# Kernel optimization log

Measured on AMD Instinct MI355X. Metric: run time of the kernel, lower is better.

Reference implementation:

```python
import jax, jax.numpy as jnp
import numpy as np
import math

H = 8        # num_heads
DK = 64      # key_dim
DV = 64      # value_dim
FACTOR = 4


def setup_inputs() -> dict:
    key = jax.random.key(0)
    B, T, S, D = 4, 2048, 2048, 512
    Dout = H * DV
    ks = jax.random.split(key, 16)
    sample_k = min(int(FACTOR * math.log(S)), S)  # = 33
    inp = {
        "x_q": jax.random.normal(ks[0], (B, T, D), jnp.float32),
        "x_k": jax.random.normal(ks[1], (B, S, D), jnp.float32),
        "x_v": jax.random.normal(ks[2], (B, S, D), jnp.float32),
        "Wq": jax.random.normal(ks[3], (D, H * DK), jnp.float32) * 0.02,
        "bq": jnp.zeros((H * DK,), jnp.float32),
        "Wk": jax.random.normal(ks[4], (D, H * DK), jnp.float32) * 0.02,
        "bk": jnp.zeros((H * DK,), jnp.float32),
        "Wv": jax.random.normal(ks[5], (D, H * DV), jnp.float32) * 0.02,
        "bv": jnp.zeros((H * DV,), jnp.float32),
        "Wo": jax.random.normal(ks[6], (H * DV, Dout), jnp.float32) * 0.02,
        "bo": jnp.zeros((Dout,), jnp.float32),
        "index_sample": jax.random.randint(ks[7], (T, sample_k), 0, S, jnp.int32),
    }
    return inp


def reference(x_q, x_k, x_v, Wq, bq, Wk, bk, Wv, bv, Wo, bo, index_sample):
    B, T, D = x_q.shape
    S = x_k.shape[1]
    u = min(int(FACTOR * math.log(T)), T)  # n_top queries kept

    q = (x_q @ Wq + bq).reshape(B, T, H, DK)
    k = (x_k @ Wk + bk).reshape(B, S, H, DK)
    v = (x_v @ Wv + bv).reshape(B, S, H, DV)

    # --- _prob_QK: sampled QK to score queries ---
    ks = k[:, index_sample]                                  # [B,T,J,H,dk]
    qk_s = jnp.einsum('bthd,btjhd->bthj', q, ks)             # [B,T,H,J]
    M = qk_s.max(-1) - qk_s.mean(-1)                         # [B,T,H]
    _, top = jax.lax.top_k(jnp.transpose(M, (0, 2, 1)), u)   # [B,H,u]

    b_idx = jnp.arange(B)[:, None, None]
    h_idx = jnp.arange(H)[None, :, None]
    q_red = q[b_idx, top, h_idx]                             # [B,H,u,dk]
    qk = jnp.einsum('bhud,bshd->bhus', q_red, k)             # [B,H,u,S]

    # --- s0: default (no mask) context = mean of values over S ---
    ctx = jnp.broadcast_to(v.mean(axis=1, keepdims=True), (B, T, H, DV))
    ctx = jnp.transpose(ctx, (0, 2, 1, 3))                   # [B,H,T,dv]

    # --- s1: scaled softmax over full keys for top queries ---
    scores = jax.nn.softmax(qk * (1.0 / math.sqrt(DK)), axis=-1)
    attn = jnp.einsum('bhus,bshd->bhud', scores, v)          # [B,H,u,dv]

    # --- scatter top-query results into context / scores ---
    ctx = ctx.at[b_idx, h_idx, top].set(attn)                # [B,H,T,dv]
    final_scores = jnp.full((B, H, T, S), 1.0 / S, dtype=scores.dtype)
    final_scores = final_scores.at[b_idx, h_idx, top].set(scores)

    out = jnp.transpose(ctx, (0, 2, 1, 3)).reshape(B, T, H * DV)
    out = out @ Wo + bo                                      # [B,T,output_dim]
    return out, final_scores
```

## Files before the change

kernel.cpp:

```cpp
#include <hip/hip_runtime.h>

typedef __attribute__((ext_vector_type(8))) short short8;
typedef __attribute__((ext_vector_type(4))) float f32x4;

constexpr int Bn  = 4;
constexpr int Tn  = 2048;
constexpr int Sn  = 2048;
constexpr int Dn  = 512;
constexpr int Hn  = 8;
constexpr int DKn = 64;
constexpr int DVn = 64;
constexpr int HDn = 512;
constexpr int SKn = 30;
constexpr int Un  = 30;
constexpr int Gu  = 2;
constexpr int NGroups = Un / Gu;
constexpr int NAttnG  = Bn * Hn * NGroups;
constexpr int NOutF   = (Bn * Tn) / 8;
constexpr int NGemm  = 768;
constexpr float kScale = 0.125f;

constexpr int NWsplit = 192;
constexpr int NVPart  = 64;
constexpr int NSampled = Bn * Tn;

constexpr int NFillG = 9216;
constexpr int NFillS = 2048;
constexpr int NFillT = 5120;
constexpr int FillRowsG = 0;
constexpr int FillRowsS = NFillG * 4;
constexpr int FillRowsT = (NFillG + NFillS) * 4;

__device__ __forceinline__ ushort bf16_rne(float x) {
  unsigned u = __float_as_uint(x);
  return (ushort)((u + 0x7fffu + ((u >> 16) & 1u)) >> 16);
}
__device__ __forceinline__ float bf16f(ushort h) {
  return __uint_as_float(((unsigned)h) << 16);
}
__device__ __forceinline__ void nt_store4(f32x4* p, f32x4 v) {
  __builtin_nontemporal_store(v, p);
}
__device__ __forceinline__ void fill_rows4_256(float* fscores, size_t r0, int tid) {
  const float c = 1.0f / Sn;
  const f32x4 c4v = {c, c, c, c};
  f32x4* fs4 = (f32x4*)fscores + r0 * (Sn / 4);
#pragma unroll
  for (int i = 0; i < 8; ++i) nt_store4(fs4 + i * 256 + tid, c4v);
}
__device__ __forceinline__ void gload_lds16(const void* g, void* lds) {
  __builtin_amdgcn_global_load_lds((const __attribute__((address_space(1))) void*)g,
                                   (__attribute__((address_space(3))) void*)lds, 16, 0, 0);
}

#define MFMA(accv, av, bv) \
  asm volatile("v_mfma_f32_16x16x32_bf16 %0, %1, %2, %0" : "+v"(accv) : "v"(av), "v"(bv))

__global__ __launch_bounds__(256) void prep_split_kernel(
    const float* __restrict__ Wq, const float* __restrict__ Wk, const float* __restrict__ Wv,
    ushort* __restrict__ WtH, ushort* __restrict__ WtL) {
  const int tid = threadIdx.x;
  const int bid = blockIdx.x;

  const int z = bid / 64, t = bid % 64;
  const int k0 = (t >> 3) * 64, n0 = (t & 7) * 64;
  const float* W = (z == 0) ? Wq : (z == 1) ? Wk : Wv;
  __shared__ float tile[64][65];
  const int r = tid >> 2, c0 = (tid & 3) * 16;
#pragma unroll
  for (int i = 0; i < 16; i += 4) {
    const float4 vv = *(const float4*)(W + (size_t)(k0 + r) * HDn + n0 + c0 + i);
    tile[r][c0 + i] = vv.x; tile[r][c0 + i + 1] = vv.y;
    tile[r][c0 + i + 2] = vv.z; tile[r][c0 + i + 3] = vv.w;
  }
  __syncthreads();
  unsigned hp[8], lp[8];
#pragma unroll
  for (int i = 0; i < 16; i += 2) {
    const float x0 = tile[c0 + i][r];
    const float x1 = tile[c0 + i + 1][r];
    const ushort h0 = bf16_rne(x0), h1 = bf16_rne(x1);
    const ushort l0 = bf16_rne(x0 - bf16f(h0)), l1 = bf16_rne(x1 - bf16f(h1));
    hp[i >> 1] = (unsigned)h0 | ((unsigned)h1 << 16);
    lp[i >> 1] = (unsigned)l0 | ((unsigned)l1 << 16);
  }
  const size_t off = (size_t)(z * 512 + n0 + r) * 512 + k0 + c0;
  *(uint4*)(WtH + off)     = make_uint4(hp[0], hp[1], hp[2], hp[3]);
  *(uint4*)(WtH + off + 8) = make_uint4(hp[4], hp[5], hp[6], hp[7]);
  *(uint4*)(WtL + off)     = make_uint4(lp[0], lp[1], lp[2], lp[3]);
  *(uint4*)(WtL + off + 8) = make_uint4(lp[4], lp[5], lp[6], lp[7]);
}

__global__ __launch_bounds__(256, 2) void gemm_fill_kernel(
    const float* __restrict__ xq, const float* __restrict__ xk, const float* __restrict__ xv,
    const ushort* __restrict__ WtH, const ushort* __restrict__ WtL,
    const float* __restrict__ bq, const float* __restrict__ bk, const float* __restrict__ bv,
    float* __restrict__ qo, float* __restrict__ ko, float* __restrict__ vo,
    float* __restrict__ fscores) {
  const int bid = blockIdx.x;
  const int tid = threadIdx.x;

  if (bid >= NGemm) {
    fill_rows4_256(fscores, (size_t)FillRowsG + (size_t)(bid - NGemm) * 4, tid);
    return;
  }

  __shared__ ushort AsH[64][32];
  __shared__ ushort AsL[64][32];
  __shared__ ushort BsH[256][32];
  __shared__ ushort BsL[256][32];

  const int z = bid >> 8;
  const int rem = bid & 255;
  const int bm = (rem >> 1) * 64;
  const int bn = (rem & 1) * 256;
  const float* X = (z == 0) ? xq : (z == 1) ? xk : xv;
  const float* bias = (z == 0) ? bq : (z == 1) ? bk : bv;
  float* Y = (z == 0) ? qo : (z == 1) ? ko : vo;

  const int lane = tid & 63;
  const int wave = tid >> 6;
  const int fr = lane & 15;
  const int gk = lane >> 4;

  const int ar = tid >> 2, ag = tid & 3;
  const float* xrow = X + (size_t)(bm + ar) * Dn + ag * 8;
  const int agq = (ag ^ ((ar >> 1) & 3)) * 8;

  const int gsrc = (lane & 3) ^ ((lane >> 3) & 3);
  const ushort* bgH = WtH + (size_t)(z * 512 + bn + wave * 64 + (lane >> 2)) * 512 + gsrc * 8;
  const ushort* bgL = WtL + (size_t)(z * 512 + bn + wave * 64 + (lane >> 2)) * 512 + gsrc * 8;
  ushort* ldsH0 = &BsH[wave * 64][0];
  ushort* ldsL0 = &BsL[wave * 64][0];

  const int gq = (gk ^ ((fr >> 1) & 3)) * 8;

  f32x4 acc[4][4];
#pragma unroll
  for (int m = 0; m < 4; ++m)
#pragma unroll
    for (int n = 0; n < 4; ++n)
#pragma unroll
      for (int j = 0; j < 4; ++j) acc[m][n][j] = 0.f;

  float4 af0 = *(const float4*)(xrow + 0);
  float4 af1 = *(const float4*)(xrow + 4);

  for (int k0 = 0; k0 < Dn; k0 += 32) {
    __syncthreads();
#pragma unroll
    for (int c = 0; c < 4; ++c) {
      gload_lds16(bgH + k0 + c * 8192, ldsH0 + c * 512);
      gload_lds16(bgL + k0 + c * 8192, ldsL0 + c * 512);
    }
    {
      float xf[8] = {af0.x, af0.y, af0.z, af0.w, af1.x, af1.y, af1.z, af1.w};
      unsigned hp[4], lp[4];
#pragma unroll
      for (int i = 0; i < 8; i += 2) {
        const ushort h0 = bf16_rne(xf[i]), h1 = bf16_rne(xf[i + 1]);
        const ushort l0 = bf16_rne(xf[i] - bf16f(h0)), l1 = bf16_rne(xf[i + 1] - bf16f(h1));
        hp[i >> 1] = (unsigned)h0 | ((unsigned)h1 << 16);
        lp[i >> 1] = (unsigned)l0 | ((unsigned)l1 << 16);
      }
      *(uint4*)&AsH[ar][agq] = make_uint4(hp[0], hp[1], hp[2], hp[3]);
      *(uint4*)&AsL[ar][agq] = make_uint4(lp[0], lp[1], lp[2], lp[3]);
    }
    if (k0 + 32 < Dn) {
      af0 = *(const float4*)(xrow + k0 + 32);
      af1 = *(const float4*)(xrow + k0 + 36);
    }
    __syncthreads();

    short8 aH[4], aL[4], bH[4], bL[4];
#pragma unroll
    for (int m = 0; m < 4; ++m) {
      aH[m] = *(const short8*)&AsH[m * 16 + fr][gq];
      aL[m] = *(const short8*)&AsL[m * 16 + fr][gq];
    }
#pragma unroll
    for (int n = 0; n < 4; ++n) {
      bH[n] = *(const short8*)&BsH[wave * 64 + n * 16 + fr][gq];
      bL[n] = *(const short8*)&BsL[wave * 64 + n * 16 + fr][gq];
    }
#pragma unroll
    for (int m = 0; m < 4; ++m)
#pragma unroll
      for (int n = 0; n < 4; ++n) {
        MFMA(acc[m][n], aH[m], bH[n]);
        MFMA(acc[m][n], aH[m], bL[n]);
        MFMA(acc[m][n], aL[m], bH[n]);
      }
  }
  asm volatile("s_nop 7\n\ts_nop 7");

  float bsv[4];
#pragma unroll
  for (int n = 0; n < 4; ++n) bsv[n] = bias[bn + wave * 64 + n * 16 + fr];
#pragma unroll
  for (int m = 0; m < 4; ++m) {
#pragma unroll
    for (int n = 0; n < 4; ++n) {
      const int col = bn + wave * 64 + n * 16 + fr;
#pragma unroll
      for (int j = 0; j < 4; ++j) {
        Y[(size_t)(bm + m * 16 + gk * 4 + j) * HDn + col] = acc[m][n][j] + bsv[n];
      }
    }
  }
}

__global__ __launch_bounds__(64) void sampled_m_kernel(
    const float* __restrict__ q, const float* __restrict__ k,
    const int* __restrict__ idxs, float* __restrict__ Mt,
    const float* __restrict__ v, float* __restrict__ vpart,
    float* __restrict__ fscores) {
  const int bid = blockIdx.x;
  const int lane = threadIdx.x;

  if (bid >= NVPart + NSampled) {
    const size_t r0 = (size_t)FillRowsS + (size_t)(bid - NVPart - NSampled) * 4;
    const float c = 1.0f / Sn;
    const f32x4 c4v = {c, c, c, c};
    f32x4* p = (f32x4*)fscores + r0 * (Sn / 4);
#pragma unroll
    for (int i = 0; i < 32; ++i) nt_store4(p + i * 64 + lane, c4v);
    return;
  }

  if (bid < NVPart) {
    const int pb = bid;
    const int b = pb >> 4, part = pb & 15;
    const float4* v4 = (const float4*)(v + (size_t)b * Sn * HDn);
    float4 a0 = make_float4(0.f, 0.f, 0.f, 0.f);
    float4 a1 = make_float4(0.f, 0.f, 0.f, 0.f);
    const int s0 = part * 128;
    for (int s = s0; s < s0 + 128; ++s) {
      const float4 x0 = v4[(size_t)s * 128 + lane * 2];
      const float4 x1 = v4[(size_t)s * 128 + lane * 2 + 1];
      a0.x += x0.x; a0.y += x0.y; a0.z += x0.z; a0.w += x0.w;
      a1.x += x1.x; a1.y += x1.y; a1.z += x1.z; a1.w += x1.w;
    }
    float4* vp4 = (float4*)vpart + (size_t)pb * 128;
    vp4[lane * 2] = a0; vp4[lane * 2 + 1] = a1;
    return;
  }

  const int inner = bid - NVPart;
  const int b = inner >> 11, t = inner & (Tn - 1);

  const int* idxt = idxs + t * SKn;
  const float* qrow = q + ((size_t)(b * Tn + t)) * HDn + lane * 8;
  const float4 qv0 = *(const float4*)qrow;
  const float4 qv1 = *(const float4*)(qrow + 4);
  const float* kb = k + (size_t)b * Sn * HDn + lane * 8;

  float mx = -1e30f, sum = 0.f;
#pragma unroll 6
  for (int j = 0; j < SKn; ++j) {
    const float* kr = kb + (size_t)idxt[j] * HDn;
    const float4 kv0 = *(const float4*)kr;
    const float4 kv1 = *(const float4*)(kr + 4);
    float p = kv0.x * qv0.x + kv0.y * qv0.y + kv0.z * qv0.z + kv0.w * qv0.w
            + kv1.x * qv1.x + kv1.y * qv1.y + kv1.z * qv1.z + kv1.w * qv1.w;
    p += __shfl_xor(p, 1);
    p += __shfl_xor(p, 2);
    p += __shfl_xor(p, 4);
    mx = fmaxf(mx, p);
    sum += p;
  }
  if ((lane & 7) == 0) {
    const int h = lane >> 3;
    Mt[((size_t)(b * Hn + h)) * Tn + t] = mx - sum * (1.0f / SKn);
  }
}

__global__ __launch_bounds__(256) void topk_vmean_base_kernel(
    const float* __restrict__ Mt, const float* __restrict__ vpart,
    const float* __restrict__ Wo, const float* __restrict__ bo,
    int* __restrict__ top, float* __restrict__ vmean, float* __restrict__ basep,
    float* __restrict__ fscores) {
  const int tid = threadIdx.x;
  const int lane = tid & 63, w = tid >> 6;

  if (blockIdx.x >= 36) {
    fill_rows4_256(fscores, (size_t)FillRowsT + (size_t)(blockIdx.x - 36) * 4, tid);
    return;
  }

  __shared__ float vals[Tn];
  __shared__ float wv[4];
  __shared__ int wi[4];
  __shared__ float4 part[256];
  __shared__ float vm[HDn];

  if (blockIdx.x < 32) {
    const int bh = blockIdx.x;
    for (int i = tid; i < Tn; i += 256) vals[i] = Mt[(size_t)bh * Tn + i];
    __syncthreads();
    for (int u = 0; u < Un; ++u) {
      float bv = -1e30f; int bi = 0x7fffffff;
      for (int i = tid; i < Tn; i += 256) {
        const float x = vals[i];
        if (x > bv) { bv = x; bi = i; }
      }
#pragma unroll
      for (int o = 1; o < 64; o <<= 1) {
        const float ov = __shfl_xor(bv, o);
        const int oi = __shfl_xor(bi, o);
        if (ov > bv || (ov == bv && oi < bi)) { bv = ov; bi = oi; }
      }
      if (lane == 0) { wv[w] = bv; wi[w] = bi; }
      __syncthreads();
      bv = wv[0]; bi = wi[0];
#pragma unroll
      for (int j = 1; j < 4; ++j) {
        if (wv[j] > bv || (wv[j] == bv && wi[j] < bi)) { bv = wv[j]; bi = wi[j]; }
      }
      if (tid == 0) { top[bh * Un + u] = bi; vals[bi] = -1e30f; }
      __syncthreads();
    }
  } else {
    const int b = blockIdx.x - 32;
    const int c4 = tid & 127, half = tid >> 7;
    float4 acc = make_float4(0.f, 0.f, 0.f, 0.f);
    for (int p = half * 8; p < half * 8 + 8; ++p) {
      const float4 x = ((const float4*)vpart)[(size_t)(b * 16 + p) * 128 + c4];
      acc.x += x.x; acc.y += x.y; acc.z += x.z; acc.w += x.w;
    }
    part[tid] = acc;
    __syncthreads();
    if (half == 0) {
      float4 a = part[c4], bpp = part[128 + c4];
      const float sc = 1.0f / Sn;
      float4 r = make_float4((a.x + bpp.x) * sc, (a.y + bpp.y) * sc,
                             (a.z + bpp.z) * sc, (a.w + bpp.w) * sc);
      *(float4*)(vm + c4 * 4) = r;
      *(float4*)(vmean + b * HDn + c4 * 4) = r;
    }
    __syncthreads();
    const float4* Wo4 = (const float4*)Wo;
    float4 acc2 = make_float4(0.f, 0.f, 0.f, 0.f);
    for (int c = half * 256; c < half * 256 + 256; ++c) {
      const float vmc = vm[c];
      const float4 wrow = Wo4[(size_t)c * 128 + c4];
      acc2.x += vmc * wrow.x; acc2.y += vmc * wrow.y;
      acc2.z += vmc * wrow.z; acc2.w += vmc * wrow.w;
    }
    __syncthreads();
    part[tid] = acc2;
    __syncthreads();
    if (half == 0) {
      float4 a = part[c4], bpp = part[128 + c4];
      const float4 bb = ((const float4*)bo)[c4];
      float4 r = make_float4(a.x + bpp.x + bb.x, a.y + bpp.y + bb.y,
                             a.z + bpp.z + bb.z, a.w + bpp.w + bb.w);
      ((float4*)basep)[b * 128 + c4] = r;
    }
  }
}

__global__ __launch_bounds__(256) void attn_out_kernel(
    const float* __restrict__ q, const float* __restrict__ k,
    const float* __restrict__ v, const float* __restrict__ vmean,
    const int* __restrict__ top, const float* __restrict__ Wo,
    const float* __restrict__ basep,
    float* __restrict__ out, float* __restrict__ fscores) {
  const int tid = threadIdx.x;
  const int bid = blockIdx.x;

  if (bid >= NAttnG) {
    const int fid = bid - NAttnG;
    const int r0 = fid * 8;
    const int b = r0 >> 11;
    const int t0 = r0 & (Tn - 1);
    __shared__ int sflag8[8];
    if (tid < 8) sflag8[tid] = 0;
    __syncthreads();
    if (tid < Hn * Un) {
      const int d = top[b * Hn * Un + tid] - t0;
      if (d >= 0 && d < 8) sflag8[d] = 1;
    }
    __syncthreads();
    const int col4 = tid & 127, rh = tid >> 7;
    const float4 bv4 = ((const float4*)basep)[b * 128 + col4];
    const f32x4 bvx = {bv4.x, bv4.y, bv4.z, bv4.w};
#pragma unroll
    for (int rp = 0; rp < 4; ++rp) {
      const int rr = rp * 2 + rh;
      float4* orow4 = (float4*)(out + (size_t)(r0 + rr) * HDn) + col4;
      if (sflag8[rr]) {
        float* p = (float*)orow4;
        atomicAdd(p + 0, bv4.x); atomicAdd(p + 1, bv4.y);
        atomicAdd(p + 2, bv4.z); atomicAdd(p + 3, bv4.w);
      } else {
        nt_store4((f32x4*)orow4, bvx);
      }
    }
    return;
  }

  const int xs = bid & 7;
  const int b = xs & 3;
  const int combo = (bid >> 3) + (xs >> 2) * 60;
  const int h = combo / NGroups;
  const int grp = combo % NGroups;
  const int bh = b * Hn + h;
  const int u0 = grp * Gu;
  const int lane = tid & 63, w = tid >> 6;

  __shared__ float qs[Gu][DKn];
  __shared__ float sc[Gu][2052];
  __shared__ float red[8];
  __shared__ int tsel[Gu];
  __shared__ float4 partv[4][Gu][16];

  if (tid < Gu) tsel[tid] = top[bh * Un + u0 + tid];
  __syncthreads();
  if (tid < Gu * DKn) {
    const int g = tid >> 6, d = tid & 63;
    qs[g][d] = q[((size_t)(b * Tn + tsel[g])) * HDn + h * DKn + d];
  }
  __syncthreads();

  const float4* k4 = (const float4*)k;
  for (int s = tid; s < Sn; s += 256) {
    const float4* krow = k4 + ((size_t)(b * Sn + s)) * 128 + h * 16;
    float acc[Gu];
#pragma unroll
    for (int g = 0; g < Gu; ++g) acc[g] = 0.f;
#pragma unroll
    for (int d4i = 0; d4i < 16; ++d4i) {
      const float4 kv = krow[d4i];
#pragma unroll
      for (int g = 0; g < Gu; ++g) {
        const float4 qv = *(const float4*)&qs[g][d4i * 4];
        acc[g] += kv.x * qv.x + kv.y * qv.y + kv.z * qv.z + kv.w * qv.w;
      }
    }
#pragma unroll
    for (int g = 0; g < Gu; ++g) sc[g][s] = acc[g] * kScale;
  }
  __syncthreads();

  float invs[Gu];
#pragma unroll
  for (int g = 0; g < Gu; ++g) {
    float lm = -1e30f;
    for (int i = tid; i < Sn; i += 256) lm = fmaxf(lm, sc[g][i]);
#pragma unroll
    for (int o = 1; o < 64; o <<= 1) lm = fmaxf(lm, __shfl_xor(lm, o));
    if (lane == 0) red[w] = lm;
    __syncthreads();
    const float mx = fmaxf(fmaxf(red[0], red[1]), fmaxf(red[2], red[3]));
    float ls = 0.f;
    for (int i = tid; i < Sn; i += 256) {
      const float e = __expf(sc[g][i] - mx);
      sc[g][i] = e;
      ls += e;
    }
#pragma unroll
    for (int o = 1; o < 64; o <<= 1) ls += __shfl_xor(ls, o);
    if (lane == 0) red[4 + w] = ls;
    __syncthreads();
    invs[g] = 1.0f / (red[4] + red[5] + red[6] + red[7]);
    __syncthreads();
  }
#pragma unroll
  for (int g = 0; g < Gu; ++g) {
    const float inv = invs[g];
    float4* scg4 = (float4*)sc[g];
    f32x4* fsrow4 = (f32x4*)(fscores + ((size_t)bh * Tn + tsel[g]) * Sn);
#pragma unroll
    for (int it = 0; it < 2; ++it) {
      const int i = it * 256 + tid;
      float4 p = scg4[i];
      p.x *= inv; p.y *= inv; p.z *= inv; p.w *= inv;
      scg4[i] = p;
      const f32x4 px = {p.x, p.y, p.z, p.w};
      nt_store4(fsrow4 + i, px);
    }
  }
  __syncthreads();

  const int d4 = lane & 15;
  const int sg = (w << 2) + (lane >> 4);
  const float4* v4 = (const float4*)v;
  float4 pacc[Gu];
#pragma unroll
  for (int g = 0; g < Gu; ++g) pacc[g] = make_float4(0.f, 0.f, 0.f, 0.f);
  for (int s = sg; s < Sn; s += 16) {
    const float4 vv = v4[((size_t)(b * Sn + s)) * 128 + h * 16 + d4];
#pragma unroll
    for (int g = 0; g < Gu; ++g) {
      const float p = sc[g][s];
      pacc[g].x += p * vv.x; pacc[g].y += p * vv.y;
      pacc[g].z += p * vv.z; pacc[g].w += p * vv.w;
    }
  }
#pragma unroll
  for (int g = 0; g < Gu; ++g) {
#pragma unroll
    for (int o = 16; o < 64; o <<= 1) {
      pacc[g].x += __shfl_xor(pacc[g].x, o);
      pacc[g].y += __shfl_xor(pacc[g].y, o);
      pacc[g].z += __shfl_xor(pacc[g].z, o);
      pacc[g].w += __shfl_xor(pacc[g].w, o);
    }
    if (lane < 16) partv[w][g][lane] = pacc[g];
  }
  __syncthreads();
  if (tid < Gu * 16) {
    const int g = tid >> 4, dd = tid & 15;
    float4 r = partv[0][g][dd];
    const float4 r1 = partv[1][g][dd], r2 = partv[2][g][dd], r3 = partv[3][g][dd];
    r.x += r1.x + r2.x + r3.x; r.y += r1.y + r2.y + r3.y;
    r.z += r1.z + r2.z + r3.z; r.w += r1.w + r2.w + r3.w;
    const float4 vm4 = ((const float4*)vmean)[bh * 16 + dd];
    r.x -= vm4.x; r.y -= vm4.y; r.z -= vm4.z; r.w -= vm4.w;
    *(float4*)&qs[g][dd * 4] = r;
  }
  __syncthreads();

  const int col4 = tid & 127, g = tid >> 7;
  const float4* Wo4 = (const float4*)Wo;
  {
    float4 a = make_float4(0.f, 0.f, 0.f, 0.f);
#pragma unroll
    for (int d = 0; d < DKn; ++d) {
      const float dv = qs[g][d];
      const float4 wrow = Wo4[(size_t)(h * DKn + d) * 128 + col4];
      a.x += dv * wrow.x; a.y += dv * wrow.y;
      a.z += dv * wrow.z; a.w += dv * wrow.w;
    }
    float* orow = out + ((size_t)(b * Tn + tsel[g])) * HDn + col4 * 4;
    atomicAdd(orow + 0, a.x); atomicAdd(orow + 1, a.y);
    atomicAdd(orow + 2, a.z); atomicAdd(orow + 3, a.w);
  }
}

extern "C" void kernel_launch(void* const* d_in, const int* in_sizes, int n_in,
                              void* d_out, int out_size, void* d_ws, size_t ws_size,
                              hipStream_t stream) {
  const float* x_q = (const float*)d_in[0];
  const float* x_k = (const float*)d_in[1];
  const float* x_v = (const float*)d_in[2];
  const float* Wq = (const float*)d_in[3];
  const float* bq = (const float*)d_in[4];
  const float* Wk = (const float*)d_in[5];
  const float* bk = (const float*)d_in[6];
  const float* Wv = (const float*)d_in[7];
  const float* bv = (const float*)d_in[8];
  const float* Wo = (const float*)d_in[9];
  const float* bo = (const float*)d_in[10];
  const int* idx = (const int*)d_in[11];

  float* out = (float*)d_out;
  float* fscores = out + (size_t)Bn * Tn * HDn;

  float* ws = (float*)d_ws;
  float* q = ws;
  float* kp = ws + (size_t)4194304;
  float* vp = ws + (size_t)8388608;
  float* Mt = ws + (size_t)12582912;
  float* vmean = ws + (size_t)12648448;
  float* basep = ws + (size_t)12650496;
  int* top = (int*)(ws + (size_t)12652544);
  float* vpart = ws + (size_t)12656640;

  char* scr = (char*)(fscores + (size_t)49152 * Sn);
  ushort* WtH = (ushort*)scr;
  ushort* WtL = WtH + (size_t)3 * 512 * 512;

  prep_split_kernel<<<NWsplit, 256, 0, stream>>>(Wq, Wk, Wv, WtH, WtL);

  gemm_fill_kernel<<<NGemm + NFillG, 256, 0, stream>>>(
      x_q, x_k, x_v, WtH, WtL, bq, bk, bv, q, kp, vp, fscores);

  sampled_m_kernel<<<NVPart + NSampled + NFillS, 64, 0, stream>>>(
      q, kp, idx, Mt, vp, vpart, fscores);

  topk_vmean_base_kernel<<<36 + NFillT, 256, 0, stream>>>(
      Mt, vpart, Wo, bo, top, vmean, basep, fscores);

  attn_out_kernel<<<NAttnG + NOutF, 256, 0, stream>>>(
      q, kp, vp, vmean, top, Wo, basep, out, fscores);
}
```

Baseline: 752.4 us.

## Use one top query per attention block and register-resident two-stage top-k

Result: slower. 786.3 us (+4.5%).

```diff
diff --git a/kernel.cpp b/kernel.cpp
--- a/kernel.cpp
+++ b/kernel.cpp
@@ -13,8 +13,7 @@
 constexpr int HDn = 512;
 constexpr int SKn = 30;
 constexpr int Un  = 30;
-constexpr int Gu  = 2;
-constexpr int NGroups = Un / Gu;
+constexpr int NGroups = Un;
 constexpr int NAttnG  = Bn * Hn * NGroups;
 constexpr int NOutF   = (Bn * Tn) / 8;
 constexpr int NGemm  = 768;
@@ -24,9 +23,9 @@
 constexpr int NVPart  = 64;
 constexpr int NSampled = Bn * Tn;
 
-constexpr int NFillG = 9216;
+constexpr int NFillG = 10240;
 constexpr int NFillS = 2048;
-constexpr int NFillT = 5120;
+constexpr int NFillT = 4096;
 constexpr int FillRowsG = 0;
 constexpr int FillRowsS = NFillG * 4;
 constexpr int FillRowsT = (NFillG + NFillS) * 4;
@@ -288,37 +287,60 @@
     return;
   }
 
-  __shared__ float vals[Tn];
-  __shared__ float wv[4];
-  __shared__ int wi[4];
+  __shared__ float cval[128];
+  __shared__ int cidx[128];
   __shared__ float4 part[256];
   __shared__ float vm[HDn];
 
   if (blockIdx.x < 32) {
     const int bh = blockIdx.x;
-    for (int i = tid; i < Tn; i += 256) vals[i] = Mt[(size_t)bh * Tn + i];
-    __syncthreads();
+    if (tid < 128) { cval[tid] = -1e30f; cidx[tid] = -1; }
+    __syncthreads();
+    const float* mrow = Mt + (size_t)bh * Tn;
+    const int base = w * 512 + lane;
+    float rv[8];
+#pragma unroll
+    for (int j = 0; j < 8; ++j) rv[j] = mrow[base + j * 64];
     for (int u = 0; u < Un; ++u) {
-      float bv = -1e30f; int bi = 0x7fffffff;
-      for (int i = tid; i < Tn; i += 256) {
-        const float x = vals[i];
-        if (x > bv) { bv = x; bi = i; }
-      }
+      float bv = rv[0]; int bj = 0;
+#pragma unroll
+      for (int j = 1; j < 8; ++j) {
+        if (rv[j] > bv) { bv = rv[j]; bj = j; }
+      }
+      int bi = base + bj * 64;
 #pragma unroll
       for (int o = 1; o < 64; o <<= 1) {
         const float ov = __shfl_xor(bv, o);
         const int oi = __shfl_xor(bi, o);
         if (ov > bv || (ov == bv && oi < bi)) { bv = ov; bi = oi; }
       }
-      if (lane == 0) { wv[w] = bv; wi[w] = bi; }
-      __syncthreads();
-      bv = wv[0]; bi = wi[0];
-#pragma unroll
-      for (int j = 1; j < 4; ++j) {
-        if (wv[j] > bv || (wv[j] == bv && wi[j] < bi)) { bv = wv[j]; bi = wi[j]; }
-      }
-      if (tid == 0) { top[bh * Un + u] = bi; vals[bi] = -1e30f; }
-      __syncthreads();
+      if (((bi >> 9) == w) && ((bi & 63) == lane)) {
+        const int bj2 = (bi >> 6) & 7;
+#pragma unroll
+        for (int j = 0; j < 8; ++j) {
+          if (j == bj2) rv[j] = -1e30f;
+        }
+      }
+      if (lane == 0) { cval[w * 32 + u] = bv; cidx[w * 32 + u] = bi; }
+    }
+    __syncthreads();
+    if (w == 0) {
+      float v0 = cval[lane], v1 = cval[64 + lane];
+      int i0 = cidx[lane], i1 = cidx[64 + lane];
+      for (int u = 0; u < Un; ++u) {
+        float bv; int bi;
+        if (v0 > v1 || (v0 == v1 && i0 < i1)) { bv = v0; bi = i0; }
+        else { bv = v1; bi = i1; }
+#pragma unroll
+        for (int o = 1; o < 64; o <<= 1) {
+          const float ov = __shfl_xor(bv, o);
+          const int oi = __shfl_xor(bi, o);
+          if (ov > bv || (ov == bv && oi < bi)) { bv = ov; bi = oi; }
+        }
+        if (i0 == bi) v0 = -1e30f;
+        if (i1 == bi) v1 = -1e30f;
+        if (lane == 0) top[bh * Un + u] = bi;
+      }
     }
   } else {
     const int b = blockIdx.x - 32;
@@ -402,75 +424,59 @@
 
   const int xs = bid & 7;
   const int b = xs & 3;
-  const int combo = (bid >> 3) + (xs >> 2) * 60;
+  const int combo = (bid >> 3) + (xs >> 2) * 120;
   const int h = combo / NGroups;
   const int grp = combo % NGroups;
   const int bh = b * Hn + h;
-  const int u0 = grp * Gu;
   const int lane = tid & 63, w = tid >> 6;
 
-  __shared__ float qs[Gu][DKn];
-  __shared__ float sc[Gu][2052];
+  __shared__ float qs[DKn];
+  __shared__ float sc[2052];
   __shared__ float red[8];
-  __shared__ int tsel[Gu];
-  __shared__ float4 partv[4][Gu][16];
-
-  if (tid < Gu) tsel[tid] = top[bh * Un + u0 + tid];
-  __syncthreads();
-  if (tid < Gu * DKn) {
-    const int g = tid >> 6, d = tid & 63;
-    qs[g][d] = q[((size_t)(b * Tn + tsel[g])) * HDn + h * DKn + d];
-  }
+  __shared__ int tsel0;
+  __shared__ float4 partv[4][16];
+
+  if (tid == 0) tsel0 = top[bh * Un + grp];
+  __syncthreads();
+  const int tsel = tsel0;
+  if (tid < DKn) qs[tid] = q[((size_t)(b * Tn + tsel)) * HDn + h * DKn + tid];
   __syncthreads();
 
   const float4* k4 = (const float4*)k;
   for (int s = tid; s < Sn; s += 256) {
     const float4* krow = k4 + ((size_t)(b * Sn + s)) * 128 + h * 16;
-    float acc[Gu];
-#pragma unroll
-    for (int g = 0; g < Gu; ++g) acc[g] = 0.f;
+    float acc = 0.f;
 #pragma unroll
     for (int d4i = 0; d4i < 16; ++d4i) {
       const float4 kv = krow[d4i];
-#pragma unroll
-      for (int g = 0; g < Gu; ++g) {
-        const float4 qv = *(const float4*)&qs[g][d4i * 4];
-        acc[g] += kv.x * qv.x + kv.y * qv.y + kv.z * qv.z + kv.w * qv.w;
-      }
-    }
-#pragma unroll
-    for (int g = 0; g < Gu; ++g) sc[g][s] = acc[g] * kScale;
-  }
-  __syncthreads();
-
-  float invs[Gu];
-#pragma unroll
-  for (int g = 0; g < Gu; ++g) {
-    float lm = -1e30f;
-    for (int i = tid; i < Sn; i += 256) lm = fmaxf(lm, sc[g][i]);
-#pragma unroll
-    for (int o = 1; o < 64; o <<= 1) lm = fmaxf(lm, __shfl_xor(lm, o));
-    if (lane == 0) red[w] = lm;
-    __syncthreads();
-    const float mx = fmaxf(fmaxf(red[0], red[1]), fmaxf(red[2], red[3]));
-    float ls = 0.f;
-    for (int i = tid; i < Sn; i += 256) {
-      const float e = __expf(sc[g][i] - mx);
-      sc[g][i] = e;
-      ls += e;
-    }
-#pragma unroll
-    for (int o = 1; o < 64; o <<= 1) ls += __shfl_xor(ls, o);
-    if (lane == 0) red[4 + w] = ls;
-    __syncthreads();
-    invs[g] = 1.0f / (red[4] + red[5] + red[6] + red[7]);
-    __syncthreads();
-  }
-#pragma unroll
-  for (int g = 0; g < Gu; ++g) {
-    const float inv = invs[g];
-    float4* scg4 = (float4*)sc[g];
-    f32x4* fsrow4 = (f32x4*)(fscores + ((size_t)bh * Tn + tsel[g]) * Sn);
+      const float4 qv = *(const float4*)&qs[d4i * 4];
+      acc += kv.x * qv.x + kv.y * qv.y + kv.z * qv.z + kv.w * qv.w;
+    }
+    sc[s] = acc * kScale;
+  }
+  __syncthreads();
+
+  float lm = -1e30f;
+  for (int i = tid; i < Sn; i += 256) lm = fmaxf(lm, sc[i]);
+#pragma unroll
+  for (int o = 1; o < 64; o <<= 1) lm = fmaxf(lm, __shfl_xor(lm, o));
+  if (lane == 0) red[w] = lm;
+  __syncthreads();
+  const float mx = fmaxf(fmaxf(red[0], red[1]), fmaxf(red[2], red[3]));
+  float ls = 0.f;
+  for (int i = tid; i < Sn; i += 256) {
+    const float e = __expf(sc[i] - mx);
+    sc[i] = e;
+    ls += e;
+  }
+#pragma unroll
+  for (int o = 1; o < 64; o <<= 1) ls += __shfl_xor(ls, o);
+  if (lane == 0) red[4 + w] = ls;
+  __syncthreads();
+  const float inv = 1.0f / (red[4] + red[5] + red[6] + red[7]);
+  {
+    float4* scg4 = (float4*)sc;
+    f32x4* fsrow4 = (f32x4*)(fscores + ((size_t)bh * Tn + tsel) * Sn);
 #pragma unroll
     for (int it = 0; it < 2; ++it) {
       const int i = it * 256 + tid;
@@ -486,54 +492,46 @@
   const int d4 = lane & 15;
   const int sg = (w << 2) + (lane >> 4);
   const float4* v4 = (const float4*)v;
-  float4 pacc[Gu];
-#pragma unroll
-  for (int g = 0; g < Gu; ++g) pacc[g] = make_float4(0.f, 0.f, 0.f, 0.f);
+  float4 pacc = make_float4(0.f, 0.f, 0.f, 0.f);
   for (int s = sg; s < Sn; s += 16) {
     const float4 vv = v4[((size_t)(b * Sn + s)) * 128 + h * 16 + d4];
-#pragma unroll
-    for (int g = 0; g < Gu; ++g) {
-      const float p = sc[g][s];
-      pacc[g].x += p * vv.x; pacc[g].y += p * vv.y;
-      pacc[g].z += p * vv.z; pacc[g].w += p * vv.w;
-    }
-  }
-#pragma unroll
-  for (int g = 0; g < Gu; ++g) {
-#pragma unroll
-    for (int o = 16; o < 64; o <<= 1) {
-      pacc[g].x += __shfl_xor(pacc[g].x, o);
-      pacc[g].y += __shfl_xor(pacc[g].y, o);
-      pacc[g].z += __shfl_xor(pacc[g].z, o);
-      pacc[g].w += __shfl_xor(pacc[g].w, o);
-    }
-    if (lane < 16) partv[w][g][lane] = pacc[g];
-  }
-  __syncthreads();
-  if (tid < Gu * 16) {
-    const int g = tid >> 4, dd = tid & 15;
-    float4 r = partv[0][g][dd];
-    const float4 r1 = partv[1][g][dd], r2 = partv[2][g][dd], r3 = partv[3][g][dd];
+    const float p = sc[s];
+    pacc.x += p * vv.x; pacc.y += p * vv.y;
+    pacc.z += p * vv.z; pacc.w += p * vv.w;
+  }
+#pragma unroll
+  for (int o = 16; o < 64; o <<= 1) {
+    pacc.x += __shfl_xor(pacc.x, o);
+    pacc.y += __shfl_xor(pacc.y, o);
+    pacc.z += __shfl_xor(pacc.z, o);
+    pacc.w += __shfl_xor(pacc.w, o);
+  }
+  if (lane < 16) partv[w][lane] = pacc;
+  __syncthreads();
+  if (tid < 16) {
+    const int dd = tid;
+    float4 r = partv[0][dd];
+    const float4 r1 = partv[1][dd], r2 = partv[2][dd], r3 = partv[3][dd];
     r.x += r1.x + r2.x + r3.x; r.y += r1.y + r2.y + r3.y;
     r.z += r1.z + r2.z + r3.z; r.w += r1.w + r2.w + r3.w;
     const float4 vm4 = ((const float4*)vmean)[bh * 16 + dd];
     r.x -= vm4.x; r.y -= vm4.y; r.z -= vm4.z; r.w -= vm4.w;
-    *(float4*)&qs[g][dd * 4] = r;
-  }
-  __syncthreads();
-
-  const int col4 = tid & 127, g = tid >> 7;
-  const float4* Wo4 = (const float4*)Wo;
-  {
+    *(float4*)&qs[dd * 4] = r;
+  }
+  __syncthreads();
+
+  if (tid < 128) {
+    const int col4 = tid;
+    const float4* Wo4 = (const float4*)Wo;
     float4 a = make_float4(0.f, 0.f, 0.f, 0.f);
 #pragma unroll
     for (int d = 0; d < DKn; ++d) {
-      const float dv = qs[g][d];
+      const float dv = qs[d];
       const float4 wrow = Wo4[(size_t)(h * DKn + d) * 128 + col4];
       a.x += dv * wrow.x; a.y += dv * wrow.y;
       a.z += dv * wrow.z; a.w += dv * wrow.w;
     }
-    float* orow = out + ((size_t)(b * Tn + tsel[g])) * HDn + col4 * 4;
+    float* orow = out + ((size_t)(b * Tn + tsel)) * HDn + col4 * 4;
     atomicAdd(orow + 0, a.x); atomicAdd(orow + 1, a.y);
     atomicAdd(orow + 2, a.z); atomicAdd(orow + 3, a.w);
   }
```
